# Performance work log

Hardware: AMD Instinct MI355X
Metric: run time of the kernel (lower is better)

Reference implementation:

```python
import jax, jax.numpy as jnp
import numpy as np

K = 16  # number of neighbors (module init arg)

def setup_inputs() -> dict:
    key = jax.random.key(0)
    M, D, N = 65536, 16, 64
    x = jax.random.normal(key, (M, D), dtype=jnp.float32)
    # equal-length segments: each point set has M // N points
    segs = jnp.full((N,), M // N, dtype=jnp.int64)
    return {"x": x, "segs": segs}

def reference(x, segs):
    # Segmented kNN graph. Segments are equal-length (static shapes for jit),
    # so the per-segment pairwise distance + top-k becomes a batched op.
    B = segs.shape[0]
    M, D = x.shape
    L = M // B  # points per segment
    pts = x.reshape(B, L, D)
    # squared euclidean distances within each segment: (B, L, L)
    sq = jnp.sum(pts * pts, axis=-1)
    d2 = sq[:, :, None] + sq[:, None, :] - 2.0 * jnp.einsum('bld,bmd->blm', pts, pts)
    # k smallest distances per point (includes self, as in DGL's knn_graph)
    _, idx = jax.lax.top_k(-d2, K)  # idx: (B, L, K), local indices within segment
    offsets = (jnp.arange(B, dtype=idx.dtype) * L)[:, None, None]
    src = (idx + offsets).reshape(-1)                      # neighbor -> global node id
    dst = (jnp.arange(L, dtype=idx.dtype)[None, :, None] + offsets)  # (B, L, 1)
    dst = jnp.broadcast_to(dst, (B, L, K)).reshape(-1)
    # edges point from k-nearest neighbors (predecessors) to each node
    return src, dst
```

## Files before the change

### kernel.cpp

```cpp
#include <hip/hip_runtime.h>
#include <stdint.h>


#define L_SEG 1024
#define M_PTS 65536

typedef __fp16 fp16x2 __attribute__((ext_vector_type(2)));
typedef __fp16 fp16x4 __attribute__((ext_vector_type(4)));
typedef float  f32x4  __attribute__((ext_vector_type(4)));

__device__ __forceinline__ uint32_t umn(uint32_t a, uint32_t b) { return a < b ? a : b; }
__device__ __forceinline__ uint32_t umx(uint32_t a, uint32_t b) { return a > b ? a : b; }

__device__ __forceinline__ void clean16(uint32_t* A) {
    #pragma unroll
    for (int j = 8; j > 0; j >>= 1) {
        #pragma unroll
        for (int i = 0; i < 16; ++i) {
            int p = i ^ j;
            if (p > i) {
                uint32_t lo = umn(A[i], A[p]);
                uint32_t hi = umx(A[i], A[p]);
                A[i] = lo; A[p] = hi;
            }
        }
    }
}

__global__ __launch_bounds__(256, 4) void knn_v6_kernel(const float* __restrict__ x,
                                                        int* __restrict__ out) {
    __shared__ __attribute__((aligned(16))) __fp16 sfrag[16384];
    __shared__ __attribute__((aligned(16))) float  ssq[L_SEG];
    __shared__ __attribute__((aligned(16))) __fp16 sq16[64 * 16];

    const int tid = threadIdx.x;
    const int b   = blockIdx.x;
    const int seg = (b & 7) * 8 + (b >> 7);
    const int qp  = (b >> 3) & 15;
    const float* xseg = x + (size_t)seg * (L_SEG * 16);
    const f32x4* gx4  = (const f32x4*)xseg;

    {
        fp16x4* fr = (fp16x4*)sfrag;
        #pragma unroll
        for (int i = 0; i < 16; ++i) {
            const int F    = i * 256 + tid;
            const int bat  = F >> 8;
            const int half = (F >> 7) & 1;
            const int e    = (F >> 1) & 63;
            const int lo   = F & 1;
            const int tt   = half * 2 + lo;
            const int g    = e >> 4;
            const int col  = e & 15;
            const int cand = bat * 64 + tt * 16 + col;
            f32x4 v = gx4[cand * 4 + g];
            union { fp16x2 h2[2]; fp16x4 h4; } u;
            u.h2[0] = __builtin_amdgcn_cvt_pkrtz(-2.0f * v[0], -2.0f * v[1]);
            u.h2[1] = __builtin_amdgcn_cvt_pkrtz(-2.0f * v[2], -2.0f * v[3]);
            fr[F] = u.h4;
        }
    }
    {
        const int c0 = tid << 2;
        #pragma unroll
        for (int c = 0; c < 4; ++c) {
            float s = 128.0f;
            #pragma unroll
            for (int d = 0; d < 4; ++d) {
                f32x4 v = gx4[(c0 + c) * 4 + d];
                s = __builtin_fmaf(v[0], v[0], s);
                s = __builtin_fmaf(v[1], v[1], s);
                s = __builtin_fmaf(v[2], v[2], s);
                s = __builtin_fmaf(v[3], v[3], s);
            }
            ssq[c0 + c] = s;
        }
    }
    if (tid < 64) {
        const f32x4* qg = gx4 + (size_t)(qp * 64 + tid) * 4;
        fp16x4* dst = (fp16x4*)(sq16 + (size_t)tid * 16);
        #pragma unroll
        for (int d = 0; d < 4; ++d) {
            f32x4 v = qg[d];
            union { fp16x2 h2[2]; fp16x4 h4; } u;
            u.h2[0] = __builtin_amdgcn_cvt_pkrtz(v[0], v[1]);
            u.h2[1] = __builtin_amdgcn_cvt_pkrtz(v[2], v[3]);
            dst[d] = u.h4;
        }
    }
    __syncthreads();

    const int lane = tid & 63;
    const int w    = tid >> 6;
    const int g    = lane >> 4;
    const int col  = lane & 15;
    const int qloc = qp * 64 + w * 16 + col;

    const fp16x4 bfrag = *(const fp16x4*)(sq16 + (size_t)(w * 16 + col) * 16 + g * 4);

    uint32_t A[16];
    #pragma unroll
    for (int i = 0; i < 16; ++i) A[i] = 0xFFFFFFFFu;

    const char* fb = (const char*)sfrag;
    const int   lb = lane * 16;

    union F2H { f32x4 v; fp16x4 h[2]; };
    F2H cur01, cur23;
    cur01.v = *(const f32x4*)(fb + lb);
    cur23.v = *(const f32x4*)(fb + 1024 + lb);

    for (int t0 = 0; t0 < 16; ++t0) {
        const int nb = ((t0 + 1) & 15) * 2048;
        F2H nxt01, nxt23;
        nxt01.v = *(const f32x4*)(fb + nb + lb);
        nxt23.v = *(const f32x4*)(fb + nb + 1024 + lb);

        uint32_t B[16];
        #pragma unroll
        for (int tt = 0; tt < 4; ++tt) {
            const int tb = t0 * 64 + tt * 16;
            const f32x4 sq = *(const f32x4*)&ssq[tb + g * 4];
            fp16x4 af = (tt < 2) ? cur01.h[tt] : cur23.h[tt - 2];
            f32x4 acc = __builtin_amdgcn_mfma_f32_16x16x16f16(af, bfrag, sq, 0, 0, 0);
            const uint32_t idxt = (uint32_t)(tb + g * 4);
            #pragma unroll
            for (int v = 0; v < 4; ++v)
                B[tt * 4 + v] = (__float_as_uint(acc[v]) & 0xFFFFFC00u) | (idxt + (uint32_t)v);
        }
        #pragma unroll
        for (int p = 1; p < 16; p <<= 1) {
            #pragma unroll
            for (int k = p; k >= 1; k >>= 1) {
                #pragma unroll
                for (int j = (k & (p - 1)); j + k < 16; j += 2 * k) {
                    #pragma unroll
                    for (int i = 0; i <= ((k - 1 < 15 - j - k) ? k - 1 : 15 - j - k); ++i) {
                        if ((i + j) / (2 * p) == (i + j + k) / (2 * p)) {
                            uint32_t lo = umn(B[i + j], B[i + j + k]);
                            uint32_t hi = umx(B[i + j], B[i + j + k]);
                            B[i + j] = lo; B[i + j + k] = hi;
                        }
                    }
                }
            }
        }
        #pragma unroll
        for (int i = 0; i < 16; ++i) A[i] = umn(A[i], B[15 - i]);
        clean16(A);

        cur01 = nxt01; cur23 = nxt23;
    }

    #pragma unroll
    for (int m = 16; m <= 32; m <<= 1) {
        uint32_t P[16];
        #pragma unroll
        for (int i = 0; i < 16; ++i) P[i] = (uint32_t)__shfl_xor((int)A[15 - i], m, 64);
        #pragma unroll
        for (int i = 0; i < 16; ++i) A[i] = umn(A[i], P[i]);
        clean16(A);
    }

    const int base = seg * L_SEG;
    const int q    = base + qloc;
    uint32_t r[4];
    #pragma unroll
    for (int v = 0; v < 4; ++v) {
        uint32_t t01 = (g & 1) ? A[4 + v]  : A[v];
        uint32_t t23 = (g & 1) ? A[12 + v] : A[8 + v];
        r[v] = (g & 2) ? t23 : t01;
    }
    int4 sv;
    sv.x = base + (int)(r[0] & 1023u);
    sv.y = base + (int)(r[1] & 1023u);
    sv.z = base + (int)(r[2] & 1023u);
    sv.w = base + (int)(r[3] & 1023u);
    ((int4*)out)[(size_t)q * 4 + g] = sv;
    ((int4*)out)[(size_t)M_PTS * 4 + (size_t)q * 4 + g] = make_int4(q, q, q, q);
}

extern "C" void kernel_launch(void* const* d_in, const int* in_sizes, int n_in,
                              void* d_out, int out_size, void* d_ws, size_t ws_size,
                              hipStream_t stream) {
    const float* x = (const float*)d_in[0];
    int* out = (int*)d_out;
    (void)d_ws; (void)ws_size;
    knn_v6_kernel<<<dim3(1024), dim3(256), 0, stream>>>(x, out);
}
```

Baseline: 92.05 us.

## Split candidate scan across two wave halves and merge top-k via LDS

Doubles the block size to 512 threads so two groups of four waves each scan half of the segment's candidate batches for the same 64 queries. The partial top-16 lists from the second half are written to shared memory and merged by the first half before output. This shortens the serial per-wave scan and adds wave-level parallelism per block, at the cost of an extra barrier, an LDS merge pass and higher register pressure under the tighter launch bounds. The software prefetch of the next batch is replaced by a 2x unrolled loop.

```diff
diff --git a/kernel.cpp b/kernel.cpp
--- a/kernel.cpp
+++ b/kernel.cpp
@@ -27,7 +27,7 @@
     }
 }
 
-__global__ __launch_bounds__(256, 4) void knn_v6_kernel(const float* __restrict__ x,
+__global__ __launch_bounds__(512, 8) void knn_v7_kernel(const float* __restrict__ x,
                                                         int* __restrict__ out) {
     __shared__ __attribute__((aligned(16))) __fp16 sfrag[16384];
     __shared__ __attribute__((aligned(16))) float  ssq[L_SEG];
@@ -43,17 +43,17 @@
     {
         fp16x4* fr = (fp16x4*)sfrag;
         #pragma unroll
-        for (int i = 0; i < 16; ++i) {
-            const int F    = i * 256 + tid;
+        for (int i = 0; i < 8; ++i) {
+            const int F    = i * 512 + tid;
             const int bat  = F >> 8;
-            const int half = (F >> 7) & 1;
+            const int hlf  = (F >> 7) & 1;
             const int e    = (F >> 1) & 63;
             const int lo   = F & 1;
-            const int tt   = half * 2 + lo;
-            const int g    = e >> 4;
-            const int col  = e & 15;
-            const int cand = bat * 64 + tt * 16 + col;
-            f32x4 v = gx4[cand * 4 + g];
+            const int tt   = hlf * 2 + lo;
+            const int gg   = e >> 4;
+            const int cc   = e & 15;
+            const int cand = bat * 64 + tt * 16 + cc;
+            f32x4 v = gx4[cand * 4 + gg];
             union { fp16x2 h2[2]; fp16x4 h4; } u;
             u.h2[0] = __builtin_amdgcn_cvt_pkrtz(-2.0f * v[0], -2.0f * v[1]);
             u.h2[1] = __builtin_amdgcn_cvt_pkrtz(-2.0f * v[2], -2.0f * v[3]);
@@ -61,9 +61,9 @@
         }
     }
     {
-        const int c0 = tid << 2;
-        #pragma unroll
-        for (int c = 0; c < 4; ++c) {
+        const int c0 = tid << 1;
+        #pragma unroll
+        for (int c = 0; c < 2; ++c) {
             float s = 128.0f;
             #pragma unroll
             for (int d = 0; d < 4; ++d) {
@@ -92,11 +92,13 @@
 
     const int lane = tid & 63;
     const int w    = tid >> 6;
+    const int qsub = w & 3;
+    const int half = w >> 2;
     const int g    = lane >> 4;
     const int col  = lane & 15;
-    const int qloc = qp * 64 + w * 16 + col;
-
-    const fp16x4 bfrag = *(const fp16x4*)(sq16 + (size_t)(w * 16 + col) * 16 + g * 4);
+    const int qloc = qp * 64 + qsub * 16 + col;
+
+    const fp16x4 bfrag = *(const fp16x4*)(sq16 + (size_t)(qsub * 16 + col) * 16 + g * 4);
 
     uint32_t A[16];
     #pragma unroll
@@ -106,22 +108,20 @@
     const int   lb = lane * 16;
 
     union F2H { f32x4 v; fp16x4 h[2]; };
-    F2H cur01, cur23;
-    cur01.v = *(const f32x4*)(fb + lb);
-    cur23.v = *(const f32x4*)(fb + 1024 + lb);
-
-    for (int t0 = 0; t0 < 16; ++t0) {
-        const int nb = ((t0 + 1) & 15) * 2048;
-        F2H nxt01, nxt23;
-        nxt01.v = *(const f32x4*)(fb + nb + lb);
-        nxt23.v = *(const f32x4*)(fb + nb + 1024 + lb);
+
+    #pragma unroll 2
+    for (int t0 = 0; t0 < 8; ++t0) {
+        const int bat = half * 8 + t0;
+        F2H c01, c23;
+        c01.v = *(const f32x4*)(fb + bat * 2048 + lb);
+        c23.v = *(const f32x4*)(fb + bat * 2048 + 1024 + lb);
 
         uint32_t B[16];
         #pragma unroll
         for (int tt = 0; tt < 4; ++tt) {
-            const int tb = t0 * 64 + tt * 16;
+            const int tb = bat * 64 + tt * 16;
             const f32x4 sq = *(const f32x4*)&ssq[tb + g * 4];
-            fp16x4 af = (tt < 2) ? cur01.h[tt] : cur23.h[tt - 2];
+            fp16x4 af = (tt < 2) ? c01.h[tt] : c23.h[tt - 2];
             f32x4 acc = __builtin_amdgcn_mfma_f32_16x16x16f16(af, bfrag, sq, 0, 0, 0);
             const uint32_t idxt = (uint32_t)(tb + g * 4);
             #pragma unroll
@@ -148,8 +148,6 @@
         #pragma unroll
         for (int i = 0; i < 16; ++i) A[i] = umn(A[i], B[15 - i]);
         clean16(A);
-
-        cur01 = nxt01; cur23 = nxt23;
     }
 
     #pragma unroll
@@ -162,22 +160,39 @@
         clean16(A);
     }
 
-    const int base = seg * L_SEG;
-    const int q    = base + qloc;
-    uint32_t r[4];
-    #pragma unroll
-    for (int v = 0; v < 4; ++v) {
-        uint32_t t01 = (g & 1) ? A[4 + v]  : A[v];
-        uint32_t t23 = (g & 1) ? A[12 + v] : A[8 + v];
-        r[v] = (g & 2) ? t23 : t01;
-    }
-    int4 sv;
-    sv.x = base + (int)(r[0] & 1023u);
-    sv.y = base + (int)(r[1] & 1023u);
-    sv.z = base + (int)(r[2] & 1023u);
-    sv.w = base + (int)(r[3] & 1023u);
-    ((int4*)out)[(size_t)q * 4 + g] = sv;
-    ((int4*)out)[(size_t)M_PTS * 4 + (size_t)q * 4 + g] = make_int4(q, q, q, q);
+    __syncthreads();
+    uint32_t (*smerge)[17] = (uint32_t (*)[17])sfrag;
+    const int qb = qsub * 16 + col;
+    if (half == 1) {
+        #pragma unroll
+        for (int v = 0; v < 4; ++v) smerge[qb][g * 4 + v] = A[g * 4 + v];
+    }
+    __syncthreads();
+    if (half == 0) {
+        uint32_t P[16];
+        #pragma unroll
+        for (int i = 0; i < 16; ++i) P[i] = smerge[qb][15 - i];
+        #pragma unroll
+        for (int i = 0; i < 16; ++i) A[i] = umn(A[i], P[i]);
+        clean16(A);
+
+        const int base = seg * L_SEG;
+        const int q    = base + qloc;
+        uint32_t r[4];
+        #pragma unroll
+        for (int v = 0; v < 4; ++v) {
+            uint32_t t01 = (g & 1) ? A[4 + v]  : A[v];
+            uint32_t t23 = (g & 1) ? A[12 + v] : A[8 + v];
+            r[v] = (g & 2) ? t23 : t01;
+        }
+        int4 sv;
+        sv.x = base + (int)(r[0] & 1023u);
+        sv.y = base + (int)(r[1] & 1023u);
+        sv.z = base + (int)(r[2] & 1023u);
+        sv.w = base + (int)(r[3] & 1023u);
+        ((int4*)out)[(size_t)q * 4 + g] = sv;
+        ((int4*)out)[(size_t)M_PTS * 4 + (size_t)q * 4 + g] = make_int4(q, q, q, q);
+    }
 }
 
 extern "C" void kernel_launch(void* const* d_in, const int* in_sizes, int n_in,
@@ -186,5 +201,5 @@
     const float* x = (const float*)d_in[0];
     int* out = (int*)d_out;
     (void)d_ws; (void)ws_size;
-    knn_v6_kernel<<<dim3(1024), dim3(256), 0, stream>>>(x, out);
+    knn_v7_kernel<<<dim3(1024), dim3(512), 0, stream>>>(x, out);
 }
```

Result: slower. 97.53 us (+6.0%).

## Pre-reduce candidate pairs before sorting and repair dropped partners in a fixup pass

Applied to the files above, without the earlier changes.

The kNN top-16 scan now takes the min of each pair of adjacent candidates before the 16-wide bitonic sort. This halves sorting work per candidate, with 128 candidates per sort step instead of 64. Any winner's dropped pair partner (index xor 1) is then recomputed with an fp16 dot product and merged back through a small shuffle-based network. The fragment shared-memory layout also becomes a plain row-major copy. This trades per-step sort cost for an extra fixup pass and different LDS access patterns.

```diff
diff --git a/kernel.cpp b/kernel.cpp
--- a/kernel.cpp
+++ b/kernel.cpp
@@ -12,24 +12,56 @@
 __device__ __forceinline__ uint32_t umn(uint32_t a, uint32_t b) { return a < b ? a : b; }
 __device__ __forceinline__ uint32_t umx(uint32_t a, uint32_t b) { return a > b ? a : b; }
 
+#define CE(arr, i, p) { uint32_t lo = umn(arr[i], arr[p]); uint32_t hi = umx(arr[i], arr[p]); arr[i] = lo; arr[p] = hi; }
+
 __device__ __forceinline__ void clean16(uint32_t* A) {
     #pragma unroll
     for (int j = 8; j > 0; j >>= 1) {
         #pragma unroll
         for (int i = 0; i < 16; ++i) {
             int p = i ^ j;
-            if (p > i) {
-                uint32_t lo = umn(A[i], A[p]);
-                uint32_t hi = umx(A[i], A[p]);
-                A[i] = lo; A[p] = hi;
+            if (p > i) CE(A, i, p);
+        }
+    }
+}
+
+__device__ __forceinline__ void sort16(uint32_t* B) {
+    #pragma unroll
+    for (int p = 1; p < 16; p <<= 1) {
+        #pragma unroll
+        for (int k = p; k >= 1; k >>= 1) {
+            #pragma unroll
+            for (int j = (k & (p - 1)); j + k < 16; j += 2 * k) {
+                #pragma unroll
+                for (int i = 0; i <= ((k - 1 < 15 - j - k) ? k - 1 : 15 - j - k); ++i) {
+                    if ((i + j) / (2 * p) == (i + j + k) / (2 * p)) CE(B, i + j, i + j + k);
+                }
             }
         }
     }
 }
 
-__global__ __launch_bounds__(256, 4) void knn_v6_kernel(const float* __restrict__ x,
+__device__ __forceinline__ void mergeg(uint32_t* A) {
+    #pragma unroll
+    for (int m = 16; m <= 32; m <<= 1) {
+        uint32_t P[16];
+        #pragma unroll
+        for (int i = 0; i < 16; ++i) P[i] = (uint32_t)__shfl_xor((int)A[15 - i], m, 64);
+        #pragma unroll
+        for (int i = 0; i < 16; ++i) A[i] = umn(A[i], P[i]);
+        clean16(A);
+    }
+}
+
+__device__ __forceinline__ uint32_t sel4(const uint32_t* A, int g, int v) {
+    uint32_t t01 = (g & 1) ? A[4 + v]  : A[v];
+    uint32_t t23 = (g & 1) ? A[12 + v] : A[8 + v];
+    return (g & 2) ? t23 : t01;
+}
+
+__global__ __launch_bounds__(256, 4) void knn_v8_kernel(const float* __restrict__ x,
                                                         int* __restrict__ out) {
-    __shared__ __attribute__((aligned(16))) __fp16 sfrag[16384];
+    __shared__ __attribute__((aligned(16))) __fp16 sc[L_SEG * 16];
     __shared__ __attribute__((aligned(16))) float  ssq[L_SEG];
     __shared__ __attribute__((aligned(16))) __fp16 sq16[64 * 16];
 
@@ -41,23 +73,14 @@
     const f32x4* gx4  = (const f32x4*)xseg;
 
     {
-        fp16x4* fr = (fp16x4*)sfrag;
+        fp16x4* scv = (fp16x4*)sc;
         #pragma unroll
         for (int i = 0; i < 16; ++i) {
-            const int F    = i * 256 + tid;
-            const int bat  = F >> 8;
-            const int half = (F >> 7) & 1;
-            const int e    = (F >> 1) & 63;
-            const int lo   = F & 1;
-            const int tt   = half * 2 + lo;
-            const int g    = e >> 4;
-            const int col  = e & 15;
-            const int cand = bat * 64 + tt * 16 + col;
-            f32x4 v = gx4[cand * 4 + g];
+            f32x4 v = gx4[tid + 256 * i];
             union { fp16x2 h2[2]; fp16x4 h4; } u;
             u.h2[0] = __builtin_amdgcn_cvt_pkrtz(-2.0f * v[0], -2.0f * v[1]);
             u.h2[1] = __builtin_amdgcn_cvt_pkrtz(-2.0f * v[2], -2.0f * v[3]);
-            fr[F] = u.h4;
+            scv[tid + 256 * i] = u.h4;
         }
     }
     {
@@ -102,80 +125,95 @@
     #pragma unroll
     for (int i = 0; i < 16; ++i) A[i] = 0xFFFFFFFFu;
 
-    const char* fb = (const char*)sfrag;
-    const int   lb = lane * 16;
-
-    union F2H { f32x4 v; fp16x4 h[2]; };
-    F2H cur01, cur23;
-    cur01.v = *(const f32x4*)(fb + lb);
-    cur23.v = *(const f32x4*)(fb + 1024 + lb);
-
-    for (int t0 = 0; t0 < 16; ++t0) {
-        const int nb = ((t0 + 1) & 15) * 2048;
-        F2H nxt01, nxt23;
-        nxt01.v = *(const f32x4*)(fb + nb + lb);
-        nxt23.v = *(const f32x4*)(fb + nb + 1024 + lb);
-
-        uint32_t B[16];
-        #pragma unroll
-        for (int tt = 0; tt < 4; ++tt) {
-            const int tb = t0 * 64 + tt * 16;
-            const f32x4 sq = *(const f32x4*)&ssq[tb + g * 4];
-            fp16x4 af = (tt < 2) ? cur01.h[tt] : cur23.h[tt - 2];
+    const __fp16* ap  = sc + (size_t)col * 16 + g * 4;
+    const float*  sqp = ssq + g * 4;
+    const uint32_t vg4 = (uint32_t)(g << 2);
+
+    #pragma unroll 2
+    for (int r = 0; r < 8; ++r) {
+        const __fp16* apr = ap  + r * 2048;
+        const float*  sqr = sqp + r * 128;
+        const uint32_t vb = vg4 + (uint32_t)(r << 7);
+        uint32_t P[16];
+        #pragma unroll
+        for (int tt = 0; tt < 8; ++tt) {
+            fp16x4 af = *(const fp16x4*)(apr + tt * 256);
+            f32x4  sq = *(const f32x4*)(sqr + tt * 16);
             f32x4 acc = __builtin_amdgcn_mfma_f32_16x16x16f16(af, bfrag, sq, 0, 0, 0);
-            const uint32_t idxt = (uint32_t)(tb + g * 4);
+            const uint32_t it = vb + (uint32_t)(tt << 4);
+            uint32_t k0 = (__float_as_uint(acc[0]) & 0xFFFFFC00u) | it;
+            uint32_t k1 = (__float_as_uint(acc[1]) & 0xFFFFFC00u) | (it + 1u);
+            uint32_t k2 = (__float_as_uint(acc[2]) & 0xFFFFFC00u) | (it + 2u);
+            uint32_t k3 = (__float_as_uint(acc[3]) & 0xFFFFFC00u) | (it + 3u);
+            P[tt * 2]     = umn(k0, k1);
+            P[tt * 2 + 1] = umn(k2, k3);
+        }
+        sort16(P);
+        #pragma unroll
+        for (int i = 0; i < 16; ++i) A[i] = umn(A[i], P[15 - i]);
+        clean16(A);
+    }
+
+    mergeg(A);
+
+    union H8 { f32x4 v[2]; fp16x2 h2[8]; };
+    H8 qq;
+    {
+        const f32x4* qf = (const f32x4*)(sq16 + (size_t)(w * 16 + col) * 16);
+        qq.v[0] = qf[0]; qq.v[1] = qf[1];
+    }
+    uint32_t B4[4];
+    #pragma unroll
+    for (int v = 0; v < 4; ++v) {
+        const uint32_t av   = sel4(A, g, v);
+        const uint32_t pidx = (av & 1023u) ^ 1u;
+        H8 cc;
+        const f32x4* cf = (const f32x4*)(sc + (size_t)pidx * 16);
+        cc.v[0] = cf[0]; cc.v[1] = cf[1];
+        float s = 0.0f;
+        #pragma unroll
+        for (int j = 0; j < 8; ++j) {
+#if __has_builtin(__builtin_amdgcn_fdot2)
+            s = __builtin_amdgcn_fdot2(cc.h2[j], qq.h2[j], s, false);
+#else
+            s = __builtin_fmaf((float)cc.h2[j][0], (float)qq.h2[j][0], s);
+            s = __builtin_fmaf((float)cc.h2[j][1], (float)qq.h2[j][1], s);
+#endif
+        }
+        const float val = s + ssq[pidx];
+        B4[v] = (__float_as_uint(val) & 0xFFFFFC00u) | pidx;
+    }
+    CE(B4, 0, 1); CE(B4, 2, 3); CE(B4, 0, 2); CE(B4, 1, 3); CE(B4, 1, 2);
+    uint32_t B8[8];
+    {
+        uint32_t Q[4];
+        #pragma unroll
+        for (int i = 0; i < 4; ++i) Q[i] = (uint32_t)__shfl_xor((int)B4[3 - i], 16, 64);
+        #pragma unroll
+        for (int i = 0; i < 4; ++i) { B8[i] = umn(B4[i], Q[i]); B8[i + 4] = umx(B4[i], Q[i]); }
+        #pragma unroll
+        for (int j = 2; j > 0; j >>= 1) {
             #pragma unroll
-            for (int v = 0; v < 4; ++v)
-                B[tt * 4 + v] = (__float_as_uint(acc[v]) & 0xFFFFFC00u) | (idxt + (uint32_t)v);
-        }
-        #pragma unroll
-        for (int p = 1; p < 16; p <<= 1) {
-            #pragma unroll
-            for (int k = p; k >= 1; k >>= 1) {
-                #pragma unroll
-                for (int j = (k & (p - 1)); j + k < 16; j += 2 * k) {
-                    #pragma unroll
-                    for (int i = 0; i <= ((k - 1 < 15 - j - k) ? k - 1 : 15 - j - k); ++i) {
-                        if ((i + j) / (2 * p) == (i + j + k) / (2 * p)) {
-                            uint32_t lo = umn(B[i + j], B[i + j + k]);
-                            uint32_t hi = umx(B[i + j], B[i + j + k]);
-                            B[i + j] = lo; B[i + j + k] = hi;
-                        }
-                    }
-                }
-            }
-        }
-        #pragma unroll
-        for (int i = 0; i < 16; ++i) A[i] = umn(A[i], B[15 - i]);
-        clean16(A);
-
-        cur01 = nxt01; cur23 = nxt23;
-    }
-
-    #pragma unroll
-    for (int m = 16; m <= 32; m <<= 1) {
-        uint32_t P[16];
-        #pragma unroll
-        for (int i = 0; i < 16; ++i) P[i] = (uint32_t)__shfl_xor((int)A[15 - i], m, 64);
-        #pragma unroll
-        for (int i = 0; i < 16; ++i) A[i] = umn(A[i], P[i]);
-        clean16(A);
-    }
+            for (int i = 0; i < 8; ++i) { int p = i ^ j; if (p > i) CE(B8, i, p); }
+        }
+    }
+    uint32_t S[16];
+    #pragma unroll
+    for (int i = 0; i < 8; ++i) S[i] = B8[i];
+    #pragma unroll
+    for (int i = 8; i < 16; ++i) S[i] = (uint32_t)__shfl_xor((int)B8[15 - i], 32, 64);
+    clean16(S);
+    #pragma unroll
+    for (int i = 0; i < 16; ++i) A[i] = umn(A[i], S[15 - i]);
+    clean16(A);
 
     const int base = seg * L_SEG;
     const int q    = base + qloc;
-    uint32_t r[4];
-    #pragma unroll
-    for (int v = 0; v < 4; ++v) {
-        uint32_t t01 = (g & 1) ? A[4 + v]  : A[v];
-        uint32_t t23 = (g & 1) ? A[12 + v] : A[8 + v];
-        r[v] = (g & 2) ? t23 : t01;
-    }
     int4 sv;
-    sv.x = base + (int)(r[0] & 1023u);
-    sv.y = base + (int)(r[1] & 1023u);
-    sv.z = base + (int)(r[2] & 1023u);
-    sv.w = base + (int)(r[3] & 1023u);
+    sv.x = base + (int)(sel4(A, g, 0) & 1023u);
+    sv.y = base + (int)(sel4(A, g, 1) & 1023u);
+    sv.z = base + (int)(sel4(A, g, 2) & 1023u);
+    sv.w = base + (int)(sel4(A, g, 3) & 1023u);
     ((int4*)out)[(size_t)q * 4 + g] = sv;
     ((int4*)out)[(size_t)M_PTS * 4 + (size_t)q * 4 + g] = make_int4(q, q, q, q);
 }
@@ -186,5 +224,5 @@
     const float* x = (const float*)d_in[0];
     int* out = (int*)d_out;
     (void)d_ws; (void)ws_size;
-    knn_v6_kernel<<<dim3(1024), dim3(256), 0, stream>>>(x, out);
-}
+    knn_v8_kernel<<<dim3(1024), dim3(256), 0, stream>>>(x, out);
+}
```

Measured after the change: 86.63 us. -5.9%, faster.
